# Kernel tuning notes

Measured on AMD Instinct MI355X. Metric: run time of the kernel, lower is better.

The kernel has to match this reference:

```python
import jax, jax.numpy as jnp
import numpy as np

HID = 256

def lstm_cell(x, h, c, Wih, Whh, bih, bhh):
    # PyTorch LSTM gate order: i, f, g, o
    g = x @ Wih.T + h @ Whh.T + bih + bhh
    i, f, gg, o = jnp.split(g, 4, axis=-1)
    c = jax.nn.sigmoid(f) * c + jax.nn.sigmoid(i) * jnp.tanh(gg)
    h = jax.nn.sigmoid(o) * jnp.tanh(c)
    return h, c

def lstm_seq(x, Wih, Whh, bih, bhh):
    # x: [B, T, D] -> outputs [B, T, H], final (h, c)
    B = x.shape[0]
    h0 = jnp.zeros((B, HID), x.dtype)
    def step(carry, xt):
        h, c = lstm_cell(xt, carry[0], carry[1], Wih, Whh, bih, bhh)
        return (h, c), h
    (h, c), ys = jax.lax.scan(step, (h0, h0), jnp.swapaxes(x, 0, 1))
    return jnp.swapaxes(ys, 0, 1), h, c

def setup_inputs():
    key = jax.random.key(0)
    B, M, H_WIN, NTH, NTW = 512, 16, 25, 64, 64
    SAL = NTH * NTW
    ks = iter(jax.random.split(key, 40))
    def U(shape):
        return jax.random.uniform(next(ks), shape, jnp.float32, -0.0625, 0.0625)
    def lstm_p(pfx, din):
        return {pfx + '_Wih': U((4 * HID, din)), pfx + '_Whh': U((4 * HID, HID)),
                pfx + '_bih': U((4 * HID,)), pfx + '_bhh': U((4 * HID,))}
    inp = {
        'encoder_position_inputs': jax.random.normal(next(ks), (B, M, 3), jnp.float32) * 0.1,
        'encoder_saliency_inputs': jax.random.uniform(next(ks), (B, M, NTH, NTW), jnp.float32),
        'decoder_position_inputs': jax.random.normal(next(ks), (B, 1, 3), jnp.float32) * 0.1,
        'decoder_saliency_inputs': jax.random.uniform(next(ks), (B, H_WIN, NTH, NTW), jnp.float32),
    }
    for pfx, din in [('pe', 3), ('se', SAL), ('fe', 2 * HID), ('pd', 3), ('sd', SAL), ('fd', 2 * HID)]:
        inp.update(lstm_p(pfx, din))
    inp['f2_W'] = U((HID, HID)); inp['f2_b'] = U((HID,))
    inp['out_W'] = U((3, HID)); inp['out_b'] = U((3,))
    return inp

def reference(encoder_position_inputs, encoder_saliency_inputs, decoder_position_inputs, decoder_saliency_inputs,
              pe_Wih, pe_Whh, pe_bih, pe_bhh, se_Wih, se_Whh, se_bih, se_bhh,
              fe_Wih, fe_Whh, fe_bih, fe_bhh, pd_Wih, pd_Whh, pd_bih, pd_bhh,
              sd_Wih, sd_Whh, sd_bih, sd_bhh, fd_Wih, fd_Whh, fd_bih, fd_bhh,
              f2_W, f2_b, out_W, out_b):
    B, M = encoder_position_inputs.shape[:2]
    SAL = encoder_saliency_inputs.shape[2] * encoder_saliency_inputs.shape[3]
    # encoder
    out_pos, h1, c1 = lstm_seq(encoder_position_inputs, pe_Wih, pe_Whh, pe_bih, pe_bhh)
    out_sal, h2, c2 = lstm_seq(encoder_saliency_inputs.reshape(B, M, SAL), se_Wih, se_Whh, se_bih, se_bhh)
    conc_enc = jnp.concatenate([out_sal, out_pos], axis=-1)
    _, hf, cf = lstm_seq(conc_enc, fe_Wih, fe_Whh, fe_bih, fe_bhh)
    # decoder: H_WINDOW single-step recurrence; fuse LSTM restarts from (hf, cf) every step
    dec_sal = decoder_saliency_inputs.reshape(B, -1, SAL)
    def step(carry, sal_t):
        inp, h1, c1, h2, c2 = carry
        h1, c1 = lstm_cell(inp, h1, c1, pd_Wih, pd_Whh, pd_bih, pd_bhh)
        h2, c2 = lstm_cell(sal_t, h2, c2, sd_Wih, sd_Whh, sd_bih, sd_bhh)
        conc = jnp.concatenate([h2, h1], axis=-1)
        hfd, _ = lstm_cell(conc, hf, cf, fd_Wih, fd_Whh, fd_bih, fd_bhh)
        fuse2 = hfd @ f2_W.T + f2_b
        delta = fuse2 @ out_W.T + out_b
        pred = inp + delta  # toPosition: orientation + motion
        return (pred, h1, c1, h2, c2), pred
    init = (decoder_position_inputs[:, 0], h1, c1, h2, c2)
    _, preds = jax.lax.scan(step, init, jnp.swapaxes(dec_sal, 0, 1))
    return jnp.swapaxes(preds, 0, 1)  # [B, H_WINDOW, 3]
```

## Files before the change

kernel.cpp:

```cpp
#include <hip/hip_runtime.h>

#define HID 256
#define BATCH 512
#define MENC 16
#define HWIN 25
#define SALSZ 4096
#define BH (BATCH * HID)

typedef __attribute__((ext_vector_type(8))) short bf16x8;
typedef __attribute__((ext_vector_type(4))) float f32x4;

__device__ __forceinline__ float sigmf(float x) { return 1.0f / (1.0f + __expf(-x)); }
__device__ __forceinline__ ushort f2bf(float f) {
    uint32_t u = __float_as_uint(f);
    return (ushort)((u + 0x7fffu + ((u >> 16) & 1u)) >> 16);
}

#define GLOAD_LDS(gp, lp) \
    __builtin_amdgcn_global_load_lds((const __attribute__((address_space(1))) void*)(gp), \
                                     (__attribute__((address_space(3))) void*)(lp), 16, 0, 0)

__device__ __forceinline__ void st_u64(void* p, unsigned long long v) {
    __hip_atomic_store((unsigned long long*)p, v, __ATOMIC_RELAXED, __HIP_MEMORY_SCOPE_AGENT);
}

__device__ __forceinline__ void gbar_arrive(unsigned int* slot)
{
    __syncthreads();
    if (threadIdx.x == 0) atomicAdd(slot, 1u);
}
__device__ __forceinline__ void gbar_wait(unsigned int* slot, unsigned int nblk)
{
    if (threadIdx.x == 0) {
        while (__hip_atomic_load(slot, __ATOMIC_RELAXED, __HIP_MEMORY_SCOPE_AGENT) < nblk)
            __builtin_amdgcn_s_sleep(1);
    }
    __syncthreads();
}

__device__ __forceinline__ void stage_wtile(const ushort* Wsrc, int ldw, int u0,
                                            ushort* lds, int lane, int wq)
{
    const int sub = lane >> 5, uu = lane & 31;
#pragma unroll
    for (int i = 0; i < 8; ++i) {
        const int row = i * 8 + wq * 2 + sub;
        const int su  = uu ^ (row & 7);
        const int gr  = (row >> 4) * HID + u0 + (row & 15);
        GLOAD_LDS(Wsrc + (size_t)gr * ldw + su * 8, lds + i * 2048 + wq * 512);
    }
}

__device__ __forceinline__ void cell_g(const ushort* hrow0, int ldh,
                                       const ushort* WsL, f32x4 acc[4], int lane)
{
    const int fr = lane & 15, fq = lane >> 4;
    const ushort* hrow = hrow0 + (size_t)fr * ldh;
#pragma unroll
    for (int ks = 0; ks < 8; ++ks) {
        const bf16x8 af = *(const bf16x8*)(hrow + ks * 32 + fq * 8);
#pragma unroll
        for (int g = 0; g < 4; ++g) {
            const int vr = g * 16 + fr;
            const bf16x8 bf = *(const bf16x8*)(WsL + vr * 256 + (((ks * 4 + fq)) ^ (vr & 7)) * 8);
            acc[g] = __builtin_amdgcn_mfma_f32_16x16x32_bf16(af, bf, acc[g], 0, 0, 0);
        }
    }
}

struct Cvt9 {
    const float* s[9];
    ushort*      d[9];
    int          end[9];
};
__global__ __launch_bounds__(256)
void cvt_multi(Cvt9 A)
{
    int i = blockIdx.x * 256 + threadIdx.x;
    if (i >= A.end[8]) return;
    int seg = 0, beg = 0;
#pragma unroll
    for (int k = 0; k < 8; ++k)
        if (i >= A.end[k]) { seg = k + 1; beg = A.end[k]; }
    const int j = i - beg;
    const float4 v = *(const float4*)(A.s[seg] + (size_t)j * 4);
    *(ushort4*)(A.d[seg] + (size_t)j * 4) = make_ushort4(f2bf(v.x), f2bf(v.y), f2bf(v.z), f2bf(v.w));
}

__device__ __forceinline__ void loadA128(const float* Ag, int lda, int tid, float4 ra[4])
{
#pragma unroll
    for (int j = 0; j < 2; ++j) {
        const int idx = j * 512 + tid;
        const int row = idx >> 3, u = idx & 7;
        const int su = (u ^ (row & 7)) * 8;
        ra[2 * j + 0] = *(const float4*)(Ag + (size_t)row * lda + su);
        ra[2 * j + 1] = *(const float4*)(Ag + (size_t)row * lda + su + 4);
    }
}
__device__ __forceinline__ void writeA128(const float4 ra[4], ushort* Al, int tid)
{
#pragma unroll
    for (int j = 0; j < 2; ++j) {
        const int idx = j * 512 + tid;
        uint4 v;
        v.x = (uint)f2bf(ra[2 * j].x) | ((uint)f2bf(ra[2 * j].y) << 16);
        v.y = (uint)f2bf(ra[2 * j].z) | ((uint)f2bf(ra[2 * j].w) << 16);
        v.z = (uint)f2bf(ra[2 * j + 1].x) | ((uint)f2bf(ra[2 * j + 1].y) << 16);
        v.w = (uint)f2bf(ra[2 * j + 1].z) | ((uint)f2bf(ra[2 * j + 1].w) << 16);
        *(uint4*)(Al + idx * 8) = v;
    }
}
__device__ __forceinline__ void stageB128(const ushort* Bg, int ldw, ushort* Bl, int tid)
{
#pragma unroll
    for (int j = 0; j < 2; ++j) {
        const int idx = j * 512 + tid;
        const int row = idx >> 3, u = idx & 7;
        const int su = (u ^ (row & 7)) * 8;
        GLOAD_LDS(Bg + (size_t)row * ldw + su, Bl + idx * 8);
    }
}

__device__ __forceinline__ void gemm128f_body(
    const float* __restrict__ A, const ushort* __restrict__ W, float* __restrict__ C,
    int lda, int ldw, int ldc, int K, int gx, int nwg, int bid,
    ushort* AsB, ushort* BsB, int tid)
{
    const int lane = tid & 63, wid = tid >> 6;
    {
        const int q = nwg >> 3, r = nwg & 7;
        const int xcd = bid & 7, o = bid >> 3;
        bid = (xcd < r) ? xcd * (q + 1) + o : r * (q + 1) + (xcd - r) * q + o;
    }
    const int m0 = (bid / gx) * 128, n0 = (bid % gx) * 128;

    const int wr = wid >> 1, wc = wid & 1;
    const int fr = lane & 15, fq = lane >> 4;

    f32x4 acc[2][4] = {};
    const int nt = K / 64;
    const float*  Ab0 = A + (size_t)m0 * lda;
    const ushort* Bb0 = W + (size_t)n0 * ldw;

    float4 ra[4];
    loadA128(Ab0, lda, tid, ra);
    stageB128(Bb0, ldw, BsB, tid);
    writeA128(ra, AsB, tid);
    loadA128(Ab0 + 64, lda, tid, ra);
    asm volatile("s_waitcnt vmcnt(4) lgkmcnt(0)" ::: "memory");
    __builtin_amdgcn_sched_barrier(0);
    __builtin_amdgcn_s_barrier();
    __builtin_amdgcn_sched_barrier(0);

    for (int t = 0; t < nt; ++t) {
        const int p = t & 1;
        const int t1 = (t + 1 < nt) ? t + 1 : nt - 1;
        const int t2 = (t + 2 < nt) ? t + 2 : nt - 1;
        stageB128(Bb0 + t1 * 64, ldw, BsB + (p ^ 1) * 8192, tid);
        writeA128(ra, AsB + (p ^ 1) * 8192, tid);
        loadA128(Ab0 + t2 * 64, lda, tid, ra);

        const ushort* Ab = AsB + p * 8192;
        const ushort* Bb = BsB + p * 8192;
#pragma unroll
        for (int ks = 0; ks < 2; ++ks) {
            bf16x8 bfr[4];
#pragma unroll
            for (int nf = 0; nf < 4; ++nf) {
                const int row = wc * 64 + nf * 16 + fr;
                bfr[nf] = *(const bf16x8*)(Bb + row * 64 + ((ks * 4 + fq) ^ (row & 7)) * 8);
            }
            bf16x8 af[2];
#pragma unroll
            for (int mf = 0; mf < 2; ++mf) {
                const int row = wr * 32 + mf * 16 + fr;
                af[mf] = *(const bf16x8*)(Ab + row * 64 + ((ks * 4 + fq) ^ (row & 7)) * 8);
            }
            __builtin_amdgcn_s_setprio(1);
#pragma unroll
            for (int mf = 0; mf < 2; ++mf)
#pragma unroll
                for (int nf = 0; nf < 4; ++nf)
                    acc[mf][nf] = __builtin_amdgcn_mfma_f32_16x16x32_bf16(
                        af[mf], bfr[nf], acc[mf][nf], 0, 0, 0);
            __builtin_amdgcn_s_setprio(0);
        }
        if (t == nt - 1) break;
        asm volatile("s_waitcnt vmcnt(4) lgkmcnt(0)" ::: "memory");
        __builtin_amdgcn_sched_barrier(0);
        __builtin_amdgcn_s_barrier();
        __builtin_amdgcn_sched_barrier(0);
    }

    const int cl = lane & 15, ch = lane >> 4;
#pragma unroll
    for (int mf = 0; mf < 2; ++mf)
#pragma unroll
        for (int nf = 0; nf < 4; ++nf)
#pragma unroll
            for (int r = 0; r < 4; ++r)
                C[(size_t)(m0 + wr * 32 + mf * 16 + ch * 4 + r) * ldc
                  + n0 + wc * 64 + nf * 16 + cl] = acc[mf][nf][r];
}

__global__ __launch_bounds__(512, 4)
void gemm128f(const float* __restrict__ A, const ushort* __restrict__ W,
              float* __restrict__ C, int gx, int nwg)
{
    __shared__ ushort As[2 * 128 * 64];
    __shared__ ushort Bs[2 * 128 * 64];
    gemm128f_body(A, W, C, SALSZ, SALSZ, 1024, SALSZ, gx, nwg, blockIdx.x, As, Bs, threadIdx.x);
}

struct EncArgs {
    const ushort *WHse, *WHpe;
    const float  *xg_se;
    const float  *enc_pos;
    const float  *se_b1, *se_b2, *pe_b1, *pe_b2;
    const float  *pe_Wih;
    ushort       *conc;
    float        *SE_C, *PE_C;
    unsigned int *bar;
};

__global__ __launch_bounds__(512, 4)
void enc_sd(EncArgs A, const float* __restrict__ sdA, const ushort* __restrict__ sdW,
            float* __restrict__ sdC)
{
    __shared__ ushort sh[34816];
    const int tid = threadIdx.x;

    if (blockIdx.x >= 128) {
        gemm128f_body(sdA, sdW, sdC, SALSZ, SALSZ, 1024, SALSZ, 8, 800,
                      (int)blockIdx.x - 128, sh, sh + 16384, tid);
        return;
    }

    const int lane = tid & 63, w = tid >> 6;
    const int role  = blockIdx.x >> 6;
    const int rem   = blockIdx.x & 63;
    const int btile = rem & 7, usup = rem >> 3;
    const int b0 = btile * 64, ub = usup * 32;
    const int usub = w & 1, bsub = w >> 1;
    const int u0t = ub + usub * 16;
    const int grp = role * 8 + btile;
    const int fr = lane & 15, fq = lane >> 4;
    const int u = u0t + fr;
    const int ul = usub * 16 + fr;
    const int coff = role ? 256 : 0;
    ushort* Ws0 = sh + usub * 16384;
    ushort (*hloc)[32] = (ushort(*)[32])(sh + 32768);

    stage_wtile(role ? A.WHpe : A.WHse, HID, u0t, Ws0, lane, bsub);

    const float* b1 = role ? A.pe_b1 : A.se_b1;
    const float* b2 = role ? A.pe_b2 : A.se_b2;
    float bias[4], wxs[4][3];
#pragma unroll
    for (int g = 0; g < 4; ++g) {
        bias[g] = b1[g * HID + u] + b2[g * HID + u];
        wxs[g][0] = wxs[g][1] = wxs[g][2] = 0.0f;
        if (role) {
            wxs[g][0] = A.pe_Wih[(g * HID + u) * 3 + 0];
            wxs[g][1] = A.pe_Wih[(g * HID + u) * 3 + 1];
            wxs[g][2] = A.pe_Wih[(g * HID + u) * 3 + 2];
        }
    }
    float c[4] = {0.f, 0.f, 0.f, 0.f};
    __syncthreads();

    for (int t = 0; t < MENC; ++t) {
        float xg[4][4];
#pragma unroll
        for (int r = 0; r < 4; ++r) {
            const int b = b0 + bsub * 16 + fq * 4 + r;
            if (role) {
                const float* xp = A.enc_pos + ((size_t)b * MENC + t) * 3;
                xg[r][0] = xp[0]; xg[r][1] = xp[1]; xg[r][2] = xp[2]; xg[r][3] = 0.f;
            } else {
#pragma unroll
                for (int g = 0; g < 4; ++g)
                    xg[r][g] = A.xg_se[((size_t)b * MENC + t) * 1024 + g * HID + u];
            }
        }
        if (t > 0) gbar_wait(A.bar + grp * MENC + (t - 1), 8);
        f32x4 acc[4] = {};
        if (t > 0)
            cell_g(A.conc + ((size_t)(t - 1) * 512 + b0 + bsub * 16) * 512 + coff, 512,
                   Ws0, acc, lane);
#pragma unroll
        for (int r = 0; r < 4; ++r) {
            const int bl = bsub * 16 + fq * 4 + r;
            const int b = b0 + bl;
            float gv[4];
#pragma unroll
            for (int g = 0; g < 4; ++g) {
                float v = acc[g][r] + bias[g];
                if (role) v += xg[r][0] * wxs[g][0] + xg[r][1] * wxs[g][1] + xg[r][2] * wxs[g][2];
                else      v += xg[r][g];
                gv[g] = v;
            }
            const float cn = sigmf(gv[1]) * c[r] + sigmf(gv[0]) * tanhf(gv[2]);
            const float hn = sigmf(gv[3]) * tanhf(cn);
            c[r] = cn;
            hloc[bl][ul] = f2bf(hn);
            if (t == MENC - 1) (role ? A.PE_C : A.SE_C)[(size_t)b * HID + u] = cn;
        }
        __syncthreads();
        {
            const int row = tid >> 3, c8 = tid & 7;
            const unsigned long long v = *(const unsigned long long*)&hloc[row][c8 * 4];
            st_u64(A.conc + ((size_t)t * 512 + b0 + row) * 512 + coff + ub + c8 * 4, v);
        }
        if (t != MENC - 1) gbar_arrive(A.bar + grp * MENC + t);
    }
}

__global__ __launch_bounds__(256)
void gemm_mfma_bt(const ushort* __restrict__ A, const ushort* __restrict__ W,
                  float* __restrict__ C, int M, int N, int K,
                  int lda, int ldw, int ldc, const float* __restrict__ rbias)
{
    __shared__ ushort As[128 * 32];
    __shared__ ushort Bs[128 * 32];
    const int t    = threadIdx.x;
    const int lane = t & 63, wid = t >> 6;
    const int m0 = blockIdx.y * 128, n0 = blockIdx.x * 128;
    const int wr = wid >> 1, wc = wid & 1;

    f32x4 acc[4][4] = {};

    const int sr = wid * 16 + (lane >> 2);
    const int su = ((lane & 3) ^ ((lane >> 3) & 3)) * 8;
    const ushort* Ag = A + (size_t)(m0 + sr) * lda + su;
    const ushort* Wg = W + (size_t)(n0 + sr) * ldw + su;
    ushort* Al = As + wid * 512;
    ushort* Bl = Bs + wid * 512;

    const int fr = lane & 15;
    const int fq = lane >> 4;
    const int sw = (fr >> 1) & 3;

    for (int k0 = 0; k0 < K; k0 += 32) {
        GLOAD_LDS(Ag,                    Al);
        GLOAD_LDS(Ag + (size_t)64 * lda, Al + 2048);
        GLOAD_LDS(Wg,                    Bl);
        GLOAD_LDS(Wg + (size_t)64 * ldw, Bl + 2048);
        Ag += 32; Wg += 32;
        __syncthreads();

        bf16x8 af[4], bfr[4];
#pragma unroll
        for (int m = 0; m < 4; ++m)
            af[m] = *(const bf16x8*)(As + (wr * 64 + m * 16 + fr) * 32 + (fq ^ sw) * 8);
#pragma unroll
        for (int n = 0; n < 4; ++n)
            bfr[n] = *(const bf16x8*)(Bs + (wc * 64 + n * 16 + fr) * 32 + (fq ^ sw) * 8);
#pragma unroll
        for (int m = 0; m < 4; ++m)
#pragma unroll
            for (int n = 0; n < 4; ++n)
                acc[m][n] = __builtin_amdgcn_mfma_f32_16x16x32_bf16(af[m], bfr[n], acc[m][n], 0, 0, 0);
        __syncthreads();
    }

    const int cl = lane & 15, ch = lane >> 4;
#pragma unroll
    for (int m = 0; m < 4; ++m)
#pragma unroll
        for (int n = 0; n < 4; ++n)
#pragma unroll
            for (int r = 0; r < 4; ++r) {
                const int mm = m0 + wr * 64 + m * 16 + ch * 4 + r;
                const int nn = n0 + wc * 64 + n * 16 + cl;
                float v = acc[m][n][r];
                if (rbias) v += rbias[(size_t)(mm & 511) * ldc + nn];
                C[(size_t)mm * ldc + nn] = v;
            }
}

__global__ __launch_bounds__(256)
void gemm_tn(const float* __restrict__ A, const float* __restrict__ W,
             const float* __restrict__ b1, const float* __restrict__ b2,
             float* __restrict__ C,
             int M, int N, int K, int lda, int ldw, int ldc)
{
    __shared__ float AsT[16][68];
    __shared__ float WsT[16][68];
    const int t  = threadIdx.x;
    const int tx = t & 15, ty = t >> 4;
    const int m0 = blockIdx.y * 64, n0 = blockIdx.x * 64;
    const int lr = t >> 2;
    const int c4 = t & 3;

    float acc[4][4];
#pragma unroll
    for (int i = 0; i < 4; ++i)
#pragma unroll
        for (int j = 0; j < 4; ++j) acc[i][j] = 0.0f;

    for (int k0 = 0; k0 < K; k0 += 16) {
        float a[4], w[4];
        const int kb = k0 + c4 * 4;
#pragma unroll
        for (int k = 0; k < 4; ++k) {
            a[k] = (kb + k < K) ? A[(size_t)(m0 + lr) * lda + kb + k] : 0.0f;
            w[k] = (kb + k < K) ? W[(size_t)(n0 + lr) * ldw + kb + k] : 0.0f;
        }
        __syncthreads();
#pragma unroll
        for (int k = 0; k < 4; ++k) {
            AsT[c4 * 4 + k][lr] = a[k];
            WsT[c4 * 4 + k][lr] = w[k];
        }
        __syncthreads();
#pragma unroll
        for (int kk = 0; kk < 16; ++kk) {
            const float4 av = *(const float4*)&AsT[kk][ty * 4];
            const float4 wv = *(const float4*)&WsT[kk][tx * 4];
            acc[0][0] += av.x * wv.x; acc[0][1] += av.x * wv.y; acc[0][2] += av.x * wv.z; acc[0][3] += av.x * wv.w;
            acc[1][0] += av.y * wv.x; acc[1][1] += av.y * wv.y; acc[1][2] += av.y * wv.z; acc[1][3] += av.y * wv.w;
            acc[2][0] += av.z * wv.x; acc[2][1] += av.z * wv.y; acc[2][2] += av.z * wv.z; acc[2][3] += av.z * wv.w;
            acc[3][0] += av.w * wv.x; acc[3][1] += av.w * wv.y; acc[3][2] += av.w * wv.z; acc[3][3] += av.w * wv.w;
        }
    }

#pragma unroll
    for (int i = 0; i < 4; ++i) {
        const int m = m0 + ty * 4 + i;
#pragma unroll
        for (int j = 0; j < 4; ++j) {
            const int n = n0 + tx * 4 + j;
            float v = acc[i][j];
            if (b1) v += b1[n];
            if (b2) v += b2[n];
            C[(size_t)m * ldc + n] = v;
        }
    }
}

struct MidArgs {
    const ushort *WHsd, *WHfe;
    const float  *xg_sd;
    const float  *xg_fe;
    const float  *sd_b1, *sd_b2, *fe_b1, *fe_b2;
    const ushort *conc;
    const float  *SE_C;
    ushort       *SDB;
    ushort       *FEB;
    float        *FEH, *FE_C;
    unsigned int *bar;
};

__global__ __launch_bounds__(1024)
void mid_chain(MidArgs A)
{
    __shared__ ushort Ws[4][64 * 256];
    __shared__ ushort hloc[64][64];
    const int tid = threadIdx.x, lane = tid & 63, w = tid >> 6;
    const int role  = blockIdx.x >> 5;
    const int rem   = blockIdx.x & 31;
    const int btile = rem & 7, usup = rem >> 3;
    const int b0 = btile * 64, ub = usup * 64;
    const int usub = w & 3, bsub = w >> 2;
    const int u0t = ub + usub * 16;
    const int grp = role * 8 + btile;
    const int fr = lane & 15, fq = lane >> 4;
    const int u = u0t + fr;
    const int ul = usub * 16 + fr;
    const int NT = role ? MENC : HWIN;

    stage_wtile(role ? A.WHfe : A.WHsd, HID, u0t, Ws[usub], lane, bsub);

    const float* b1 = role ? A.fe_b1 : A.sd_b1;
    const float* b2 = role ? A.fe_b2 : A.sd_b2;
    float bias[4];
#pragma unroll
    for (int g = 0; g < 4; ++g) bias[g] = b1[g * HID + u] + b2[g * HID + u];

    float c[4];
#pragma unroll
    for (int r = 0; r < 4; ++r) {
        const int b = b0 + bsub * 16 + fq * 4 + r;
        c[r] = role ? 0.0f : A.SE_C[(size_t)b * HID + u];
    }
    __syncthreads();

    for (int t = 0; t < NT; ++t) {
        float xg[4][4];
#pragma unroll
        for (int r = 0; r < 4; ++r) {
            const int b = b0 + bsub * 16 + fq * 4 + r;
#pragma unroll
            for (int g = 0; g < 4; ++g)
                xg[r][g] = role ? A.xg_fe[((size_t)t * 512 + b) * 1024 + g * HID + u]
                                : A.xg_sd[((size_t)b * HWIN + t) * 1024 + g * HID + u];
        }
        if (t > 0) gbar_wait(A.bar + grp * HWIN + (t - 1), 4);
        f32x4 acc[4] = {};
        if (role == 0) {
            if (t == 0) cell_g(A.conc + ((size_t)15 * 512 + b0 + bsub * 16) * 512, 512,
                               Ws[usub], acc, lane);
            else        cell_g(A.SDB + ((size_t)(t - 1) * 512 + b0 + bsub * 16) * HID, HID,
                               Ws[usub], acc, lane);
        } else if (t > 0) {
            cell_g(A.FEB + ((size_t)(t - 1) * BATCH + b0 + bsub * 16) * HID, HID,
                   Ws[usub], acc, lane);
        }
#pragma unroll
        for (int r = 0; r < 4; ++r) {
            const int bl = bsub * 16 + fq * 4 + r;
            const int b = b0 + bl;
            float gv[4];
#pragma unroll
            for (int g = 0; g < 4; ++g)
                gv[g] = acc[g][r] + bias[g] + xg[r][g];
            const float cn = sigmf(gv[1]) * c[r] + sigmf(gv[0]) * tanhf(gv[2]);
            const float hn = sigmf(gv[3]) * tanhf(cn);
            c[r] = cn;
            hloc[bl][ul] = f2bf(hn);
            if (role == 1 && t == MENC - 1) {
                A.FEH[(size_t)b * HID + u] = hn;
                A.FE_C[(size_t)b * HID + u] = cn;
            }
        }
        __syncthreads();
        {
            const int row = tid >> 4, c8 = tid & 15;
            const unsigned long long v = *(const unsigned long long*)&hloc[row][c8 * 4];
            ushort* dst = role ? (A.FEB + ((size_t)t * BATCH + b0 + row) * 256 + ub + c8 * 4)
                               : (A.SDB + ((size_t)t * 512 + b0 + row) * 256 + ub + c8 * 4);
            st_u64(dst, v);
        }
        if (t != NT - 1) gbar_arrive(A.bar + grp * HWIN + t);
    }
}

struct DecArgs {
    const ushort *WHpd;
    const ushort *WFDh;
    const ushort *peF;
    const float  *PE_C, *FE_C;
    const float  *xh2;
    const float  *pd_b1, *pd_b2, *pd_Wih;
    const float  *G, *c3, *dec_pos;
    ushort       *H1;
    float        *DELTA;
    float        *out;
    unsigned int *bar;
};

__global__ __launch_bounds__(512)
void dec_chain(DecArgs A)
{
    __shared__ ushort Wpd[2][64 * 256], Wfd[2][64 * 256];
    __shared__ ushort hloc[64][32];
    __shared__ float pred_lds[192];
    const int tid = threadIdx.x, lane = tid & 63, w = tid >> 6;
    const int btile = blockIdx.x & 7, usup = blockIdx.x >> 3;
    const int b0 = btile * 64, ub = usup * 32;
    const int usub = w & 1, bsub = w >> 1;
    const int u0t = ub + usub * 16;
    const int fr = lane & 15, fq = lane >> 4;
    const int u = u0t + fr;
    const int ul = usub * 16 + fr;
    unsigned int* bars = A.bar + btile * 2 * HWIN;

    stage_wtile(A.WHpd, HID, u0t, Wpd[usub], lane, bsub);
    stage_wtile(A.WFDh, 512, u0t, Wfd[usub], lane, bsub);

    float pdb[4], wxs[4][3], cf[4], c1[4], Gu[3];
#pragma unroll
    for (int g = 0; g < 4; ++g) {
        pdb[g] = A.pd_b1[g * HID + u] + A.pd_b2[g * HID + u];
        wxs[g][0] = A.pd_Wih[(g * HID + u) * 3 + 0];
        wxs[g][1] = A.pd_Wih[(g * HID + u) * 3 + 1];
        wxs[g][2] = A.pd_Wih[(g * HID + u) * 3 + 2];
    }
#pragma unroll
    for (int r = 0; r < 4; ++r) {
        const int b = b0 + bsub * 16 + fq * 4 + r;
        c1[r] = A.PE_C[(size_t)b * HID + u];
        cf[r] = A.FE_C[(size_t)b * HID + u];
    }
    Gu[0] = A.G[0 * HID + u]; Gu[1] = A.G[1 * HID + u]; Gu[2] = A.G[2 * HID + u];
    const float c3r = (tid < 192) ? A.c3[tid % 3] : 0.0f;
    if (tid < 192) pred_lds[tid] = A.dec_pos[(size_t)(b0 + tid / 3) * 3 + tid % 3];
    __syncthreads();

    for (int t = 0; t < HWIN; ++t) {
        f32x4 acc[4] = {};
        if (t == 0) cell_g(A.peF + (size_t)(b0 + bsub * 16) * 512, 512, Wpd[usub], acc, lane);
        else        cell_g(A.H1 + ((size_t)(t - 1) * BATCH + b0 + bsub * 16) * HID, HID,
                           Wpd[usub], acc, lane);
        if (t > 0) {
            gbar_wait(bars + 2 * (t - 1) + 1, 8);
            if (tid < 192) {
                pred_lds[tid] += A.DELTA[((size_t)(t - 1) * 512 + b0 + tid / 3) * 3 + tid % 3] + c3r;
                if (usup == 0)
                    A.out[((size_t)(b0 + tid / 3) * HWIN + (t - 1)) * 3 + tid % 3] = pred_lds[tid];
            }
            __syncthreads();
        }
#pragma unroll
        for (int r = 0; r < 4; ++r) {
            const int bl = bsub * 16 + fq * 4 + r;
            const float x0 = pred_lds[bl * 3 + 0];
            const float x1 = pred_lds[bl * 3 + 1];
            const float x2 = pred_lds[bl * 3 + 2];
            float gv[4];
#pragma unroll
            for (int g = 0; g < 4; ++g)
                gv[g] = acc[g][r] + pdb[g] + x0 * wxs[g][0] + x1 * wxs[g][1] + x2 * wxs[g][2];
            const float cn = sigmf(gv[1]) * c1[r] + sigmf(gv[0]) * tanhf(gv[2]);
            const float hn = sigmf(gv[3]) * tanhf(cn);
            c1[r] = cn;
            hloc[bl][ul] = f2bf(hn);
        }
        __syncthreads();
        {
            const int row = tid >> 3, c8 = tid & 7;
            const unsigned long long v = *(const unsigned long long*)&hloc[row][c8 * 4];
            st_u64(A.H1 + ((size_t)t * BATCH + b0 + row) * 256 + ub + c8 * 4, v);
        }
        gbar_arrive(bars + 2 * t);
        float xh[4][4];
#pragma unroll
        for (int r = 0; r < 4; ++r) {
            const int b = b0 + bsub * 16 + fq * 4 + r;
#pragma unroll
            for (int g = 0; g < 4; ++g)
                xh[r][g] = A.xh2[((size_t)t * 512 + b) * 1024 + g * HID + u];
        }
        gbar_wait(bars + 2 * t, 8);
        {
            f32x4 accB[4] = {};
            cell_g(A.H1 + ((size_t)t * BATCH + b0 + bsub * 16) * HID, HID,
                   Wfd[usub], accB, lane);
#pragma unroll
            for (int r = 0; r < 4; ++r) {
                const int b = b0 + bsub * 16 + fq * 4 + r;
                float gv[4];
#pragma unroll
                for (int g = 0; g < 4; ++g)
                    gv[g] = accB[g][r] + xh[r][g];
                const float cn = sigmf(gv[1]) * cf[r] + sigmf(gv[0]) * tanhf(gv[2]);
                const float hn = sigmf(gv[3]) * tanhf(cn);
                float p0 = hn * Gu[0], p1 = hn * Gu[1], p2 = hn * Gu[2];
#pragma unroll
                for (int s = 1; s < 16; s <<= 1) {
                    p0 += __shfl_xor(p0, s);
                    p1 += __shfl_xor(p1, s);
                    p2 += __shfl_xor(p2, s);
                }
                if (fr == 0) {
                    float* d = A.DELTA + ((size_t)t * 512 + b) * 3;
                    atomicAdd(d + 0, p0); atomicAdd(d + 1, p1); atomicAdd(d + 2, p2);
                }
            }
        }
        gbar_arrive(bars + 2 * t + 1);
    }
    gbar_wait(bars + 2 * (HWIN - 1) + 1, 8);
    if (tid < 192) {
        pred_lds[tid] += A.DELTA[((size_t)(HWIN - 1) * 512 + b0 + tid / 3) * 3 + tid % 3] + c3r;
        if (usup == 0)
            A.out[((size_t)(b0 + tid / 3) * HWIN + (HWIN - 1)) * 3 + tid % 3] = pred_lds[tid];
    }
}

__global__ __launch_bounds__(256)
void precompute_G(const float* __restrict__ f2W, const float* __restrict__ f2b,
                  const float* __restrict__ outW, const float* __restrict__ outb,
                  float* __restrict__ G, float* __restrict__ c3)
{
    const int k = threadIdx.x;
    float g0 = 0.f, g1 = 0.f, g2 = 0.f;
    for (int n = 0; n < HID; ++n) {
        const float w = f2W[n * HID + k];
        g0 += outW[n] * w;
        g1 += outW[HID + n] * w;
        g2 += outW[2 * HID + n] * w;
    }
    G[k] = g0; G[HID + k] = g1; G[2 * HID + k] = g2;
    if (k < 3) {
        float s = outb[k];
        for (int n = 0; n < HID; ++n) s += outW[k * HID + n] * f2b[n];
        c3[k] = s;
    }
}

extern "C" void kernel_launch(void* const* d_in, const int* in_sizes, int n_in,
                              void* d_out, int out_size, void* d_ws, size_t ws_size,
                              hipStream_t stream)
{
    (void)in_sizes; (void)n_in; (void)out_size; (void)ws_size;
    const float* enc_pos = (const float*)d_in[0];
    const float* enc_sal = (const float*)d_in[1];
    const float* dec_pos = (const float*)d_in[2];
    const float* dec_sal = (const float*)d_in[3];
    const float *pe_Wih = (const float*)d_in[4],  *pe_Whh = (const float*)d_in[5],
                *pe_bih = (const float*)d_in[6],  *pe_bhh = (const float*)d_in[7];
    const float *se_Wih = (const float*)d_in[8],  *se_Whh = (const float*)d_in[9],
                *se_bih = (const float*)d_in[10], *se_bhh = (const float*)d_in[11];
    const float *fe_Wih = (const float*)d_in[12], *fe_Whh = (const float*)d_in[13],
                *fe_bih = (const float*)d_in[14], *fe_bhh = (const float*)d_in[15];
    const float *pd_Wih = (const float*)d_in[16], *pd_Whh = (const float*)d_in[17],
                *pd_bih = (const float*)d_in[18], *pd_bhh = (const float*)d_in[19];
    const float *sd_Wih = (const float*)d_in[20], *sd_Whh = (const float*)d_in[21],
                *sd_bih = (const float*)d_in[22], *sd_bhh = (const float*)d_in[23];
    const float *fd_Wih = (const float*)d_in[24], *fd_Whh = (const float*)d_in[25],
                *fd_bih = (const float*)d_in[26], *fd_bhh = (const float*)d_in[27];
    const float *f2_W = (const float*)d_in[28], *f2_b = (const float*)d_in[29];
    const float *out_W = (const float*)d_in[30], *out_b = (const float*)d_in[31];
    float* out = (float*)d_out;
    float* ws  = (float*)d_ws;

    size_t off = 0;
    float* XG_SE = ws + off; off += (size_t)8192 * 1024;
    float* XG_FE = ws + off; off += (size_t)8192 * 1024;
    float* BIG   = ws + off; off += (size_t)12800 * 1024;
    float* BIG2  = ws + off; off += (size_t)12800 * 1024;
    float* GBIAS = ws + off; off += (size_t)BATCH * 1024;
    float* PE_C  = ws + off; off += BH;
    float* SE_C  = ws + off; off += BH;
    float* FE_C  = ws + off; off += BH;
    float* FEH   = ws + off; off += BH;
    float* Gm    = ws + off; off += 1024;
    float* C3    = ws + off; off += 8;
    float* DELTA = ws + off; off += (size_t)HWIN * BATCH * 3 + 64;
    unsigned int* BAR = (unsigned int*)(ws + off); off += 1280;
    ushort* WSE  = (ushort*)(ws + off); off += ((size_t)1024 * 4096) / 2;
    ushort* WSD  = (ushort*)(ws + off); off += ((size_t)1024 * 4096) / 2;
    ushort* WFE  = (ushort*)(ws + off); off += ((size_t)1024 * 512) / 2;
    ushort* WFD  = (ushort*)(ws + off); off += ((size_t)1024 * 512) / 2;
    ushort* WHpe = (ushort*)(ws + off); off += ((size_t)1024 * 256) / 2;
    ushort* WHse = (ushort*)(ws + off); off += ((size_t)1024 * 256) / 2;
    ushort* WHfe = (ushort*)(ws + off); off += ((size_t)1024 * 256) / 2;
    ushort* WHsd = (ushort*)(ws + off); off += ((size_t)1024 * 256) / 2;
    ushort* WHpd = (ushort*)(ws + off); off += ((size_t)1024 * 256) / 2;
    ushort* CONC = (ushort*)(ws + off); off += ((size_t)MENC * 512 * 512) / 2;
    ushort* SDB  = (ushort*)(ws + off); off += ((size_t)HWIN * BH) / 2;
    ushort* FEB  = (ushort*)(ws + off); off += ((size_t)MENC * BH) / 2;
    ushort* H1   = (ushort*)(ws + off); off += ((size_t)HWIN * BH) / 2;

    hipMemsetAsync(DELTA, 0, ((size_t)HWIN * BATCH * 3 + 64 + 1280) * 4, stream);

    auto mgemm = [&](const ushort* A, const ushort* W, float* C,
                     int M, int N, int K, int lda, int ldw, int ldc, const float* rb) {
        gemm_mfma_bt<<<dim3(N / 128, M / 128), 256, 0, stream>>>(A, W, C, M, N, K, lda, ldw, ldc, rb);
    };

    {
        Cvt9 a;
        const float* srcs[9] = { se_Wih, sd_Wih, fe_Wih, fd_Wih, pe_Whh, se_Whh, fe_Whh, sd_Whh, pd_Whh };
        ushort*      dsts[9] = { WSE,    WSD,    WFE,    WFD,    WHpe,   WHse,   WHfe,   WHsd,   WHpd };
        const int    n4s[9]  = { 1024*4096/4, 1024*4096/4, 1024*512/4, 1024*512/4,
                                 1024*256/4, 1024*256/4, 1024*256/4, 1024*256/4, 1024*256/4 };
        int acc9 = 0;
        for (int i = 0; i < 9; ++i) { a.s[i] = srcs[i]; a.d[i] = dsts[i]; acc9 += n4s[i]; a.end[i] = acc9; }
        cvt_multi<<<(acc9 + 255) / 256, 256, 0, stream>>>(a);
    }
    precompute_G<<<1, 256, 0, stream>>>(f2_W, f2_b, out_W, out_b, Gm, C3);

    gemm128f<<<512, 512, 0, stream>>>(enc_sal, WSE, XG_SE, 8, 512);

    {
        EncArgs a;
        a.WHse = WHse; a.WHpe = WHpe; a.xg_se = XG_SE; a.enc_pos = enc_pos;
        a.se_b1 = se_bih; a.se_b2 = se_bhh; a.pe_b1 = pe_bih; a.pe_b2 = pe_bhh;
        a.pe_Wih = pe_Wih; a.conc = CONC; a.SE_C = SE_C; a.PE_C = PE_C;
        a.bar = BAR;
        enc_sd<<<928, 512, 0, stream>>>(a, dec_sal, WSD, BIG);
    }

    mgemm(CONC, WFE, XG_FE, 8192, 1024, 512, 512, 512, 1024, nullptr);

    {
        MidArgs a;
        a.WHsd = WHsd; a.WHfe = WHfe; a.xg_sd = BIG; a.xg_fe = XG_FE;
        a.sd_b1 = sd_bih; a.sd_b2 = sd_bhh; a.fe_b1 = fe_bih; a.fe_b2 = fe_bhh;
        a.conc = CONC; a.SE_C = SE_C; a.SDB = SDB; a.FEB = FEB;
        a.FEH = FEH; a.FE_C = FE_C; a.bar = BAR + 256;
        mid_chain<<<64, 1024, 0, stream>>>(a);
    }

    gemm_tn<<<dim3(16, 8), 256, 0, stream>>>(FEH, fd_Whh, fd_bih, fd_bhh, GBIAS,
                                             BATCH, 1024, HID, HID, HID, 1024);
    mgemm(SDB, WFD, BIG2, 12800, 1024, HID, HID, 512, 1024, GBIAS);

    {
        DecArgs a;
        a.WHpd = WHpd; a.WFDh = WFD + 256;
        a.peF = CONC + ((size_t)15 * 512) * 512 + 256;
        a.PE_C = PE_C; a.FE_C = FE_C; a.xh2 = BIG2;
        a.pd_b1 = pd_bih; a.pd_b2 = pd_bhh; a.pd_Wih = pd_Wih;
        a.G = Gm; a.c3 = C3; a.dec_pos = dec_pos;
        a.H1 = H1; a.DELTA = DELTA; a.out = out; a.bar = BAR + 656;
        dec_chain<<<64, 512, 0, stream>>>(a);
    }
}
```

Before: 1.033 ms.

## Fuse input-projection GEMMs into recurrent chain kernels with per-timestep completion flags

The standalone fe input-projection GEMM is merged into the mid recurrence kernel, and the fd input GEMM into the decoder recurrence kernel. Extra workgroups compute GEMM tiles and bump per-timestep done counters, and the recurrent workgroups spin on those counters before consuming each timestep. The aim is to overlap GEMM work with the latency-bound recurrences and remove kernel launch boundaries. The mid recurrence is also re-split from 64 blocks of 1024 threads to 128 blocks of 512 threads. This relies on every recurrent block being co-resident with the GEMM blocks, or the spin-waits can deadlock.

```diff
diff --git a/kernel.cpp b/kernel.cpp
--- a/kernel.cpp
+++ b/kernel.cpp
@@ -22,6 +22,9 @@
 
 __device__ __forceinline__ void st_u64(void* p, unsigned long long v) {
     __hip_atomic_store((unsigned long long*)p, v, __ATOMIC_RELAXED, __HIP_MEMORY_SCOPE_AGENT);
+}
+__device__ __forceinline__ void st_f32(float* p, float v) {
+    __hip_atomic_store(p, v, __ATOMIC_RELAXED, __HIP_MEMORY_SCOPE_AGENT);
 }
 
 __device__ __forceinline__ void gbar_arrive(unsigned int* slot)
@@ -211,6 +214,82 @@
     __shared__ ushort As[2 * 128 * 64];
     __shared__ ushort Bs[2 * 128 * 64];
     gemm128f_body(A, W, C, SALSZ, SALSZ, 1024, SALSZ, gx, nwg, blockIdx.x, As, Bs, threadIdx.x);
+}
+
+__device__ __forceinline__ void gemm128b_body(
+    const ushort* __restrict__ A, const ushort* __restrict__ W, float* __restrict__ C,
+    int lda, int ldw, int ldc, int K, int gx, int nwg, int bid,
+    const float* __restrict__ rbias, unsigned int* flag,
+    ushort* AsB, ushort* BsB, int tid)
+{
+    const int lane = tid & 63, wid = tid >> 6;
+    {
+        const int q = nwg >> 3, r = nwg & 7;
+        const int xcd = bid & 7, o = bid >> 3;
+        bid = (xcd < r) ? xcd * (q + 1) + o : r * (q + 1) + (xcd - r) * q + o;
+    }
+    const int m0 = (bid / gx) * 128, n0 = (bid % gx) * 128;
+
+    const int wr = wid >> 1, wc = wid & 1;
+    const int fr = lane & 15, fq = lane >> 4;
+
+    f32x4 acc[2][4] = {};
+    const int nt = K / 64;
+    const ushort* Ab0 = A + (size_t)m0 * lda;
+    const ushort* Bb0 = W + (size_t)n0 * ldw;
+
+    stageB128(Ab0, lda, AsB, tid);
+    stageB128(Bb0, ldw, BsB, tid);
+    __syncthreads();
+
+    for (int t = 0; t < nt; ++t) {
+        const int p = t & 1;
+        if (t + 1 < nt) {
+            stageB128(Ab0 + (t + 1) * 64, lda, AsB + (p ^ 1) * 8192, tid);
+            stageB128(Bb0 + (t + 1) * 64, ldw, BsB + (p ^ 1) * 8192, tid);
+        }
+        const ushort* Ab = AsB + p * 8192;
+        const ushort* Bb = BsB + p * 8192;
+#pragma unroll
+        for (int ks = 0; ks < 2; ++ks) {
+            bf16x8 bfr[4];
+#pragma unroll
+            for (int nf = 0; nf < 4; ++nf) {
+                const int row = wc * 64 + nf * 16 + fr;
+                bfr[nf] = *(const bf16x8*)(Bb + row * 64 + ((ks * 4 + fq) ^ (row & 7)) * 8);
+            }
+            bf16x8 af[2];
+#pragma unroll
+            for (int mf = 0; mf < 2; ++mf) {
+                const int row = wr * 32 + mf * 16 + fr;
+                af[mf] = *(const bf16x8*)(Ab + row * 64 + ((ks * 4 + fq) ^ (row & 7)) * 8);
+            }
+#pragma unroll
+            for (int mf = 0; mf < 2; ++mf)
+#pragma unroll
+                for (int nf = 0; nf < 4; ++nf)
+                    acc[mf][nf] = __builtin_amdgcn_mfma_f32_16x16x32_bf16(
+                        af[mf], bfr[nf], acc[mf][nf], 0, 0, 0);
+        }
+        if (t == nt - 1) break;
+        __syncthreads();
+    }
+
+    const int cl = lane & 15, ch = lane >> 4;
+#pragma unroll
+    for (int mf = 0; mf < 2; ++mf)
+#pragma unroll
+        for (int nf = 0; nf < 4; ++nf)
+#pragma unroll
+            for (int r = 0; r < 4; ++r) {
+                const int mm = m0 + wr * 32 + mf * 16 + ch * 4 + r;
+                const int nn = n0 + wc * 64 + nf * 16 + cl;
+                float v = acc[mf][nf][r];
+                if (rbias) v += rbias[(size_t)(mm & 511) * ldc + nn];
+                st_f32(C + (size_t)mm * ldc + nn, v);
+            }
+    __syncthreads();
+    if (tid == 0) atomicAdd(flag + (m0 >> 9), 1u);
 }
 
 struct EncArgs {
@@ -317,129 +396,6 @@
     }
 }
 
-__global__ __launch_bounds__(256)
-void gemm_mfma_bt(const ushort* __restrict__ A, const ushort* __restrict__ W,
-                  float* __restrict__ C, int M, int N, int K,
-                  int lda, int ldw, int ldc, const float* __restrict__ rbias)
-{
-    __shared__ ushort As[128 * 32];
-    __shared__ ushort Bs[128 * 32];
-    const int t    = threadIdx.x;
-    const int lane = t & 63, wid = t >> 6;
-    const int m0 = blockIdx.y * 128, n0 = blockIdx.x * 128;
-    const int wr = wid >> 1, wc = wid & 1;
-
-    f32x4 acc[4][4] = {};
-
-    const int sr = wid * 16 + (lane >> 2);
-    const int su = ((lane & 3) ^ ((lane >> 3) & 3)) * 8;
-    const ushort* Ag = A + (size_t)(m0 + sr) * lda + su;
-    const ushort* Wg = W + (size_t)(n0 + sr) * ldw + su;
-    ushort* Al = As + wid * 512;
-    ushort* Bl = Bs + wid * 512;
-
-    const int fr = lane & 15;
-    const int fq = lane >> 4;
-    const int sw = (fr >> 1) & 3;
-
-    for (int k0 = 0; k0 < K; k0 += 32) {
-        GLOAD_LDS(Ag,                    Al);
-        GLOAD_LDS(Ag + (size_t)64 * lda, Al + 2048);
-        GLOAD_LDS(Wg,                    Bl);
-        GLOAD_LDS(Wg + (size_t)64 * ldw, Bl + 2048);
-        Ag += 32; Wg += 32;
-        __syncthreads();
-
-        bf16x8 af[4], bfr[4];
-#pragma unroll
-        for (int m = 0; m < 4; ++m)
-            af[m] = *(const bf16x8*)(As + (wr * 64 + m * 16 + fr) * 32 + (fq ^ sw) * 8);
-#pragma unroll
-        for (int n = 0; n < 4; ++n)
-            bfr[n] = *(const bf16x8*)(Bs + (wc * 64 + n * 16 + fr) * 32 + (fq ^ sw) * 8);
-#pragma unroll
-        for (int m = 0; m < 4; ++m)
-#pragma unroll
-            for (int n = 0; n < 4; ++n)
-                acc[m][n] = __builtin_amdgcn_mfma_f32_16x16x32_bf16(af[m], bfr[n], acc[m][n], 0, 0, 0);
-        __syncthreads();
-    }
-
-    const int cl = lane & 15, ch = lane >> 4;
-#pragma unroll
-    for (int m = 0; m < 4; ++m)
-#pragma unroll
-        for (int n = 0; n < 4; ++n)
-#pragma unroll
-            for (int r = 0; r < 4; ++r) {
-                const int mm = m0 + wr * 64 + m * 16 + ch * 4 + r;
-                const int nn = n0 + wc * 64 + n * 16 + cl;
-                float v = acc[m][n][r];
-                if (rbias) v += rbias[(size_t)(mm & 511) * ldc + nn];
-                C[(size_t)mm * ldc + nn] = v;
-            }
-}
-
-__global__ __launch_bounds__(256)
-void gemm_tn(const float* __restrict__ A, const float* __restrict__ W,
-             const float* __restrict__ b1, const float* __restrict__ b2,
-             float* __restrict__ C,
-             int M, int N, int K, int lda, int ldw, int ldc)
-{
-    __shared__ float AsT[16][68];
-    __shared__ float WsT[16][68];
-    const int t  = threadIdx.x;
-    const int tx = t & 15, ty = t >> 4;
-    const int m0 = blockIdx.y * 64, n0 = blockIdx.x * 64;
-    const int lr = t >> 2;
-    const int c4 = t & 3;
-
-    float acc[4][4];
-#pragma unroll
-    for (int i = 0; i < 4; ++i)
-#pragma unroll
-        for (int j = 0; j < 4; ++j) acc[i][j] = 0.0f;
-
-    for (int k0 = 0; k0 < K; k0 += 16) {
-        float a[4], w[4];
-        const int kb = k0 + c4 * 4;
-#pragma unroll
-        for (int k = 0; k < 4; ++k) {
-            a[k] = (kb + k < K) ? A[(size_t)(m0 + lr) * lda + kb + k] : 0.0f;
-            w[k] = (kb + k < K) ? W[(size_t)(n0 + lr) * ldw + kb + k] : 0.0f;
-        }
-        __syncthreads();
-#pragma unroll
-        for (int k = 0; k < 4; ++k) {
-            AsT[c4 * 4 + k][lr] = a[k];
-            WsT[c4 * 4 + k][lr] = w[k];
-        }
-        __syncthreads();
-#pragma unroll
-        for (int kk = 0; kk < 16; ++kk) {
-            const float4 av = *(const float4*)&AsT[kk][ty * 4];
-            const float4 wv = *(const float4*)&WsT[kk][tx * 4];
-            acc[0][0] += av.x * wv.x; acc[0][1] += av.x * wv.y; acc[0][2] += av.x * wv.z; acc[0][3] += av.x * wv.w;
-            acc[1][0] += av.y * wv.x; acc[1][1] += av.y * wv.y; acc[1][2] += av.y * wv.z; acc[1][3] += av.y * wv.w;
-            acc[2][0] += av.z * wv.x; acc[2][1] += av.z * wv.y; acc[2][2] += av.z * wv.z; acc[2][3] += av.z * wv.w;
-            acc[3][0] += av.w * wv.x; acc[3][1] += av.w * wv.y; acc[3][2] += av.w * wv.z; acc[3][3] += av.w * wv.w;
-        }
-    }
-
-#pragma unroll
-    for (int i = 0; i < 4; ++i) {
-        const int m = m0 + ty * 4 + i;
-#pragma unroll
-        for (int j = 0; j < 4; ++j) {
-            const int n = n0 + tx * 4 + j;
-            float v = acc[i][j];
-            if (b1) v += b1[n];
-            if (b2) v += b2[n];
-            C[(size_t)m * ldc + n] = v;
-        }
-    }
-}
-
 struct MidArgs {
     const ushort *WHsd, *WHfe;
     const float  *xg_sd;
@@ -451,27 +407,38 @@
     ushort       *FEB;
     float        *FEH, *FE_C;
     unsigned int *bar;
+    unsigned int *fe_done;
 };
 
-__global__ __launch_bounds__(1024)
-void mid_chain(MidArgs A)
-{
-    __shared__ ushort Ws[4][64 * 256];
-    __shared__ ushort hloc[64][64];
-    const int tid = threadIdx.x, lane = tid & 63, w = tid >> 6;
-    const int role  = blockIdx.x >> 5;
-    const int rem   = blockIdx.x & 31;
+__global__ __launch_bounds__(512, 4)
+void mid_fe(MidArgs A, const ushort* __restrict__ feA, const ushort* __restrict__ feW,
+            float* __restrict__ feC)
+{
+    __shared__ ushort sh[34816];
+    const int tid = threadIdx.x;
+
+    if (blockIdx.x >= 128) {
+        gemm128b_body(feA, feW, feC, 512, 512, 1024, 512, 8, 512,
+                      (int)blockIdx.x - 128, nullptr, A.fe_done, sh, sh + 16384, tid);
+        return;
+    }
+
+    const int lane = tid & 63, w = tid >> 6;
+    const int role  = blockIdx.x >> 6;
+    const int rem   = blockIdx.x & 63;
     const int btile = rem & 7, usup = rem >> 3;
-    const int b0 = btile * 64, ub = usup * 64;
-    const int usub = w & 3, bsub = w >> 2;
+    const int b0 = btile * 64, ub = usup * 32;
+    const int usub = w & 1, bsub = w >> 1;
     const int u0t = ub + usub * 16;
     const int grp = role * 8 + btile;
     const int fr = lane & 15, fq = lane >> 4;
     const int u = u0t + fr;
     const int ul = usub * 16 + fr;
     const int NT = role ? MENC : HWIN;
-
-    stage_wtile(role ? A.WHfe : A.WHsd, HID, u0t, Ws[usub], lane, bsub);
+    ushort* Ws0 = sh + usub * 16384;
+    ushort (*hloc)[32] = (ushort(*)[32])(sh + 32768);
+
+    stage_wtile(role ? A.WHfe : A.WHsd, HID, u0t, Ws0, lane, bsub);
 
     const float* b1 = role ? A.fe_b1 : A.sd_b1;
     const float* b2 = role ? A.fe_b2 : A.sd_b2;
@@ -488,6 +455,7 @@
     __syncthreads();
 
     for (int t = 0; t < NT; ++t) {
+        if (role) gbar_wait(A.fe_done + t, 32);
         float xg[4][4];
 #pragma unroll
         for (int r = 0; r < 4; ++r) {
@@ -497,16 +465,16 @@
                 xg[r][g] = role ? A.xg_fe[((size_t)t * 512 + b) * 1024 + g * HID + u]
                                 : A.xg_sd[((size_t)b * HWIN + t) * 1024 + g * HID + u];
         }
-        if (t > 0) gbar_wait(A.bar + grp * HWIN + (t - 1), 4);
+        if (t > 0) gbar_wait(A.bar + grp * HWIN + (t - 1), 8);
         f32x4 acc[4] = {};
         if (role == 0) {
             if (t == 0) cell_g(A.conc + ((size_t)15 * 512 + b0 + bsub * 16) * 512, 512,
-                               Ws[usub], acc, lane);
+                               Ws0, acc, lane);
             else        cell_g(A.SDB + ((size_t)(t - 1) * 512 + b0 + bsub * 16) * HID, HID,
-                               Ws[usub], acc, lane);
+                               Ws0, acc, lane);
         } else if (t > 0) {
             cell_g(A.FEB + ((size_t)(t - 1) * BATCH + b0 + bsub * 16) * HID, HID,
-                   Ws[usub], acc, lane);
+                   Ws0, acc, lane);
         }
 #pragma unroll
         for (int r = 0; r < 4; ++r) {
@@ -527,13 +495,73 @@
         }
         __syncthreads();
         {
-            const int row = tid >> 4, c8 = tid & 15;
+            const int row = tid >> 3, c8 = tid & 7;
             const unsigned long long v = *(const unsigned long long*)&hloc[row][c8 * 4];
             ushort* dst = role ? (A.FEB + ((size_t)t * BATCH + b0 + row) * 256 + ub + c8 * 4)
                                : (A.SDB + ((size_t)t * 512 + b0 + row) * 256 + ub + c8 * 4);
             st_u64(dst, v);
         }
         if (t != NT - 1) gbar_arrive(A.bar + grp * HWIN + t);
+    }
+}
+
+__global__ __launch_bounds__(256)
+void gemm_tn(const float* __restrict__ A, const float* __restrict__ W,
+             const float* __restrict__ b1, const float* __restrict__ b2,
+             float* __restrict__ C,
+             int M, int N, int K, int lda, int ldw, int ldc)
+{
+    __shared__ float AsT[16][68];
+    __shared__ float WsT[16][68];
+    const int t  = threadIdx.x;
+    const int tx = t & 15, ty = t >> 4;
+    const int m0 = blockIdx.y * 64, n0 = blockIdx.x * 64;
+    const int lr = t >> 2;
+    const int c4 = t & 3;
+
+    float acc[4][4];
+#pragma unroll
+    for (int i = 0; i < 4; ++i)
+#pragma unroll
+        for (int j = 0; j < 4; ++j) acc[i][j] = 0.0f;
+
+    for (int k0 = 0; k0 < K; k0 += 16) {
+        float a[4], w[4];
+        const int kb = k0 + c4 * 4;
+#pragma unroll
+        for (int k = 0; k < 4; ++k) {
+            a[k] = (kb + k < K) ? A[(size_t)(m0 + lr) * lda + kb + k] : 0.0f;
+            w[k] = (kb + k < K) ? W[(size_t)(n0 + lr) * ldw + kb + k] : 0.0f;
+        }
+        __syncthreads();
+#pragma unroll
+        for (int k = 0; k < 4; ++k) {
+            AsT[c4 * 4 + k][lr] = a[k];
+            WsT[c4 * 4 + k][lr] = w[k];
+        }
+        __syncthreads();
+#pragma unroll
+        for (int kk = 0; kk < 16; ++kk) {
+            const float4 av = *(const float4*)&AsT[kk][ty * 4];
+            const float4 wv = *(const float4*)&WsT[kk][tx * 4];
+            acc[0][0] += av.x * wv.x; acc[0][1] += av.x * wv.y; acc[0][2] += av.x * wv.z; acc[0][3] += av.x * wv.w;
+            acc[1][0] += av.y * wv.x; acc[1][1] += av.y * wv.y; acc[1][2] += av.y * wv.z; acc[1][3] += av.y * wv.w;
+            acc[2][0] += av.z * wv.x; acc[2][1] += av.z * wv.y; acc[2][2] += av.z * wv.z; acc[2][3] += av.z * wv.w;
+            acc[3][0] += av.w * wv.x; acc[3][1] += av.w * wv.y; acc[3][2] += av.w * wv.z; acc[3][3] += av.w * wv.w;
+        }
+    }
+
+#pragma unroll
+    for (int i = 0; i < 4; ++i) {
+        const int m = m0 + ty * 4 + i;
+#pragma unroll
+        for (int j = 0; j < 4; ++j) {
+            const int n = n0 + tx * 4 + j;
+            float v = acc[i][j];
+            if (b1) v += b1[n];
+            if (b2) v += b2[n];
+            C[(size_t)m * ldc + n] = v;
+        }
     }
 }
 
@@ -549,15 +577,28 @@
     float        *DELTA;
     float        *out;
     unsigned int *bar;
+    unsigned int *xh2_done;
 };
 
 __global__ __launch_bounds__(512)
-void dec_chain(DecArgs A)
-{
-    __shared__ ushort Wpd[2][64 * 256], Wfd[2][64 * 256];
-    __shared__ ushort hloc[64][32];
-    __shared__ float pred_lds[192];
-    const int tid = threadIdx.x, lane = tid & 63, w = tid >> 6;
+void dec_xh2(DecArgs A, const ushort* __restrict__ xA, const ushort* __restrict__ xW,
+             float* __restrict__ xC, const float* __restrict__ xrb)
+{
+    __shared__ ushort sh[68096];
+    const int tid = threadIdx.x;
+
+    if (blockIdx.x >= 64) {
+        gemm128b_body(xA, xW, xC, 256, 512, 1024, 256, 8, 800,
+                      (int)blockIdx.x - 64, xrb, A.xh2_done, sh, sh + 16384, tid);
+        return;
+    }
+
+    ushort* Wpd0 = sh;
+    ushort* Wfd0 = sh + 32768;
+    ushort (*hloc)[32] = (ushort(*)[32])(sh + 65536);
+    float* pred_lds = (float*)(sh + 67584);
+
+    const int lane = tid & 63, w = tid >> 6;
     const int btile = blockIdx.x & 7, usup = blockIdx.x >> 3;
     const int b0 = btile * 64, ub = usup * 32;
     const int usub = w & 1, bsub = w >> 1;
@@ -567,8 +608,8 @@
     const int ul = usub * 16 + fr;
     unsigned int* bars = A.bar + btile * 2 * HWIN;
 
-    stage_wtile(A.WHpd, HID, u0t, Wpd[usub], lane, bsub);
-    stage_wtile(A.WFDh, 512, u0t, Wfd[usub], lane, bsub);
+    stage_wtile(A.WHpd, HID, u0t, Wpd0 + usub * 16384, lane, bsub);
+    stage_wtile(A.WFDh, 512, u0t, Wfd0 + usub * 16384, lane, bsub);
 
     float pdb[4], wxs[4][3], cf[4], c1[4], Gu[3];
 #pragma unroll
@@ -591,9 +632,10 @@
 
     for (int t = 0; t < HWIN; ++t) {
         f32x4 acc[4] = {};
-        if (t == 0) cell_g(A.peF + (size_t)(b0 + bsub * 16) * 512, 512, Wpd[usub], acc, lane);
+        if (t == 0) cell_g(A.peF + (size_t)(b0 + bsub * 16) * 512, 512,
+                           Wpd0 + usub * 16384, acc, lane);
         else        cell_g(A.H1 + ((size_t)(t - 1) * BATCH + b0 + bsub * 16) * HID, HID,
-                           Wpd[usub], acc, lane);
+                           Wpd0 + usub * 16384, acc, lane);
         if (t > 0) {
             gbar_wait(bars + 2 * (t - 1) + 1, 8);
             if (tid < 192) {
@@ -625,6 +667,7 @@
             st_u64(A.H1 + ((size_t)t * BATCH + b0 + row) * 256 + ub + c8 * 4, v);
         }
         gbar_arrive(bars + 2 * t);
+        gbar_wait(A.xh2_done + t, 32);
         float xh[4][4];
 #pragma unroll
         for (int r = 0; r < 4; ++r) {
@@ -637,7 +680,7 @@
         {
             f32x4 accB[4] = {};
             cell_g(A.H1 + ((size_t)t * BATCH + b0 + bsub * 16) * HID, HID,
-                   Wfd[usub], accB, lane);
+                   Wfd0 + usub * 16384, accB, lane);
 #pragma unroll
             for (int r = 0; r < 4; ++r) {
                 const int b = b0 + bsub * 16 + fq * 4 + r;
@@ -745,12 +788,10 @@
     ushort* FEB  = (ushort*)(ws + off); off += ((size_t)MENC * BH) / 2;
     ushort* H1   = (ushort*)(ws + off); off += ((size_t)HWIN * BH) / 2;
 
+    unsigned int* FE_DONE  = BAR + 1100;
+    unsigned int* XH2_DONE = BAR + 1128;
+
     hipMemsetAsync(DELTA, 0, ((size_t)HWIN * BATCH * 3 + 64 + 1280) * 4, stream);
-
-    auto mgemm = [&](const ushort* A, const ushort* W, float* C,
-                     int M, int N, int K, int lda, int ldw, int ldc, const float* rb) {
-        gemm_mfma_bt<<<dim3(N / 128, M / 128), 256, 0, stream>>>(A, W, C, M, N, K, lda, ldw, ldc, rb);
-    };
 
     {
         Cvt9 a;
@@ -775,20 +816,17 @@
         enc_sd<<<928, 512, 0, stream>>>(a, dec_sal, WSD, BIG);
     }
 
-    mgemm(CONC, WFE, XG_FE, 8192, 1024, 512, 512, 512, 1024, nullptr);
-
     {
         MidArgs a;
         a.WHsd = WHsd; a.WHfe = WHfe; a.xg_sd = BIG; a.xg_fe = XG_FE;
         a.sd_b1 = sd_bih; a.sd_b2 = sd_bhh; a.fe_b1 = fe_bih; a.fe_b2 = fe_bhh;
         a.conc = CONC; a.SE_C = SE_C; a.SDB = SDB; a.FEB = FEB;
-        a.FEH = FEH; a.FE_C = FE_C; a.bar = BAR + 256;
-        mid_chain<<<64, 1024, 0, stream>>>(a);
+        a.FEH = FEH; a.FE_C = FE_C; a.bar = BAR + 256; a.fe_done = FE_DONE;
+        mid_fe<<<640, 512, 0, stream>>>(a, CONC, WFE, XG_FE);
     }
 
     gemm_tn<<<dim3(16, 8), 256, 0, stream>>>(FEH, fd_Whh, fd_bih, fd_bhh, GBIAS,
                                              BATCH, 1024, HID, HID, HID, 1024);
-    mgemm(SDB, WFD, BIG2, 12800, 1024, HID, HID, 512, 1024, GBIAS);
 
     {
         DecArgs a;
@@ -798,6 +836,7 @@
         a.pd_b1 = pd_bih; a.pd_b2 = pd_bhh; a.pd_Wih = pd_Wih;
         a.G = Gm; a.c3 = C3; a.dec_pos = dec_pos;
         a.H1 = H1; a.DELTA = DELTA; a.out = out; a.bar = BAR + 656;
-        dec_chain<<<64, 512, 0, stream>>>(a);
-    }
-}
+        a.xh2_done = XH2_DONE;
+        dec_xh2<<<864, 512, 0, stream>>>(a, SDB, WFD, BIG2, GBIAS);
+    }
+}
```

New measurement: 964.1 us. 1.07x faster.
